# Kernel optimization log

Measured on AMD Instinct MI355X. Metric: run time of the kernel, lower is better.

The kernel has to match this reference:

```python
import jax, jax.numpy as jnp
import numpy as np
from jax import lax

N = 4096        # number of nodes (= number of hyperedges)
F_DIM = 256     # feature_dim
E_DIM = 128     # embed_dim
K = 9           # hardcoded k_neig in forward


def setup_inputs() -> dict:
    key = jax.random.key(0)
    ks = jax.random.split(key, 10)
    x = jax.random.normal(ks[0], (N, F_DIM), jnp.float32)
    # distance/similarity matrix; continuous values avoid argsort tie ambiguity
    XY_Adj = jax.random.uniform(ks[1], (N, N), jnp.float32)

    def unif(k, shape, fan_out):  # torch HGNN_conv init: U(-1/sqrt(out), 1/sqrt(out))
        s = 1.0 / np.sqrt(fan_out)
        return jax.random.uniform(k, shape, jnp.float32, -s, s)

    W10 = unif(ks[2], (F_DIM, E_DIM), E_DIM); b10 = unif(ks[3], (E_DIM,), E_DIM)
    W11 = unif(ks[4], (E_DIM, E_DIM), E_DIM); b11 = unif(ks[5], (E_DIM,), E_DIM)
    W20 = unif(ks[6], (E_DIM, E_DIM), E_DIM); b20 = unif(ks[7], (E_DIM,), E_DIM)
    W21 = unif(ks[8], (E_DIM, F_DIM), F_DIM); b21 = unif(ks[9], (F_DIM,), F_DIM)
    return {"x": x, "XY_Adj": XY_Adj,
            "W10": W10, "b10": b10, "W11": W11, "b11": b11,
            "W20": W20, "b20": b20, "W21": W21, "b21": b21}


def _build_G(dis, k):
    """Vectorized construct_H_with_KNN_from_distance + _generate_G_from_H.
    Picks the k LARGEST entries per row (original does reversed argsort),
    forces the center node into its own hyperedge, builds binary H [N,N]
    (rows=nodes, cols=hyperedges), then G = DV^-1/2 H DE^-1 H^T DV^-1/2 (W=I)."""
    n = dis.shape[0]
    centers = jnp.arange(n)
    dis = jnp.where(jnp.eye(n, dtype=bool), 0.0, dis)  # zero the diagonal
    _, idx = lax.top_k(dis, k)                         # [N, k] descending per row
    has_center = (idx == centers[:, None]).any(axis=1)
    idx = idx.at[:, k - 1].set(jnp.where(has_center, idx[:, k - 1], centers))
    H = jnp.zeros((n, n), dis.dtype).at[idx, centers[:, None]].set(1.0)
    DV = H.sum(axis=1)                                 # node degrees (>=1)
    DE = H.sum(axis=0)                                 # hyperedge degrees (=k)
    dv2 = DV ** -0.5
    left = dv2[:, None] * H * (1.0 / DE)[None, :]      # DV^-1/2 H DE^-1
    G = left @ (H.T * dv2[None, :])                    # ... H^T DV^-1/2
    return G


def _hgnn(x, G, W1, b1, W2, b2):
    # HGNN: relu(G(xW1+b1)) -> dropout (identity in eval) -> G(hW2+b2)
    h = jax.nn.relu(G @ (x @ W1 + b1))
    return G @ (h @ W2 + b2)


def reference(x, XY_Adj, W10, b10, W11, b11, W20, b20, W21, b21):
    G = _build_G(XY_Adj, K)
    x1 = jax.nn.relu(_hgnn(x, G, W10, b10, W11, b11))
    x2 = jax.nn.relu(_hgnn(x1, G, W20, b20, W21, b21))
    return (x, x1, x2)
```

## Files before the change

kernel.cpp:

```cpp
#include <hip/hip_runtime.h>

#define N_NODES 4096
#define KNN 9
#define CAPS 128
#define CAPE 32
#define THRESH 0.99f

__device__ __forceinline__ bool vi_greater(float av, int aj, float bv, int bj) {
  return (av > bv) || (av == bv && aj < bj);
}

__global__ void init_kernel(int* __restrict__ cur, int* __restrict__ elist) {
  int gid = blockIdx.x * blockDim.x + threadIdx.x;
  if (gid < N_NODES) cur[gid] = 0;
  for (int t = gid; t < N_NODES * CAPE; t += gridDim.x * blockDim.x)
    elist[t] = 0;
}

__global__ __launch_bounds__(256) void topk_kernel(const float* __restrict__ dis,
                                                   int* __restrict__ idx,
                                                   int* __restrict__ cur,
                                                   int* __restrict__ elist) {
  __shared__ float sval[4 * CAPS];
  __shared__ int   sidx[4 * CAPS];
  const int lane = threadIdx.x & 63;
  const int wv = threadIdx.x >> 6;
  const int row = blockIdx.x * 4 + wv;
  const float4* r4 = reinterpret_cast<const float4*>(dis + (size_t)row * N_NODES);
  float* wval = sval + wv * CAPS;
  int*   widx = sidx + wv * CAPS;
  const unsigned long long lmask = (1ull << lane) - 1;

  int n = 0;
#pragma unroll 4
  for (int t = 0; t < 16; ++t) {
    float4 f4 = r4[t * 64 + lane];
    float vals[4] = {f4.x, f4.y, f4.z, f4.w};
    int cb = (t * 64 + lane) * 4;
#pragma unroll
    for (int q = 0; q < 4; ++q) {
      int cc = cb + q;
      bool pred = (vals[q] > THRESH) && (cc != row);
      unsigned long long m = __ballot(pred);
      if (pred) {
        int p = n + __popcll(m & lmask);
        if (p < CAPS) { wval[p] = vals[q]; widx[p] = cc; }
      }
      n += __popcll(m);
    }
  }
  __syncthreads();

  int outj[KNN];
  if (n >= 8 && n <= CAPS) {
    float v0 = -3.0e38f, v1 = -3.0e38f;
    int c0 = 0x7fffffff, c1 = 0x7fffffff;
    if (lane < n)      { v0 = wval[lane];      c0 = widx[lane]; }
    if (lane + 64 < n) { v1 = wval[lane + 64]; c1 = widx[lane + 64]; }
#pragma unroll
    for (int rnd = 0; rnd < 8; ++rnd) {
      bool first = vi_greater(v0, c0, v1, c1);
      float mv = first ? v0 : v1;
      int   mc = first ? c0 : c1;
#pragma unroll
      for (int d = 1; d < 64; d <<= 1) {
        float ov = __shfl_xor(mv, d);
        int   oc = __shfl_xor(mc, d);
        if (vi_greater(ov, oc, mv, mc)) { mv = ov; mc = oc; }
      }
      outj[rnd] = mc;
      if (c0 == mc) v0 = -3.3e38f;
      if (c1 == mc) v1 = -3.3e38f;
    }
    outj[8] = row;
  } else {
    const float* r = dis + (size_t)row * N_NODES;
    float v[9]; int ji[9];
#pragma unroll
    for (int t = 0; t < 9; ++t) { v[t] = -3.0e38f; ji[t] = 0x7fffffff; }
    for (int t = 0; t < 64; ++t) {
      int cc = t * 64 + lane;
      float val = (cc == row) ? 0.0f : r[cc];
      if (vi_greater(val, cc, v[8], ji[8])) {
        v[8] = val; ji[8] = cc;
#pragma unroll
        for (int s = 8; s > 0; --s) {
          if (vi_greater(v[s], ji[s], v[s-1], ji[s-1])) {
            float tv = v[s]; v[s] = v[s-1]; v[s-1] = tv;
            int tj = ji[s]; ji[s] = ji[s-1]; ji[s-1] = tj;
          }
        }
      }
    }
    bool has_center = false;
#pragma unroll
    for (int rnd = 0; rnd < 9; ++rnd) {
      float mv = v[0]; int mj = ji[0];
#pragma unroll
      for (int d = 1; d < 64; d <<= 1) {
        float ov = __shfl_xor(mv, d);
        int   oj = __shfl_xor(mj, d);
        if (vi_greater(ov, oj, mv, mj)) { mv = ov; mj = oj; }
      }
      outj[rnd] = mj;
      has_center = has_center || (mj == row);
      if (ji[0] == mj) {
#pragma unroll
        for (int s = 0; s < 8; ++s) { v[s] = v[s+1]; ji[s] = ji[s+1]; }
        v[8] = -3.0e38f; ji[8] = 0x7fffffff;
      }
    }
    if (!has_center) outj[8] = row;
  }

  if (lane < KNN) {
    int j = outj[lane];
    idx[row * KNN + lane] = j;
    int p = atomicAdd(&cur[j], 1);
    if (p < CAPE) elist[j * CAPE + p] = row;
  }
}

template<int F>
__global__ __launch_bounds__(F) void edge_gather(const float* __restrict__ Y,
                                                 const int* __restrict__ idx,
                                                 const int* __restrict__ DV,
                                                 float* __restrict__ Z) {
  __shared__ int er[KNN];
  __shared__ float ew[KNN];
  int e = blockIdx.x;
  if (threadIdx.x < KNN) {
    int r = idx[e * KNN + threadIdx.x];
    er[threadIdx.x] = r;
    ew[threadIdx.x] = rsqrtf((float)DV[r]);
  }
  __syncthreads();
  int f = threadIdx.x;
  float acc = 0.f;
#pragma unroll
  for (int j = 0; j < KNN; ++j)
    acc = fmaf(ew[j], Y[(size_t)er[j] * F + f], acc);
  Z[(size_t)e * F + f] = acc * (1.0f / 9.0f);
}

template<int KD>
__device__ __forceinline__ float node_acc(const float* __restrict__ Z,
                                          const int* __restrict__ elist,
                                          int i, int f, int cnt) {
  const int4* el4 = reinterpret_cast<const int4*>(elist + i * CAPE);
  int4 ea = el4[0], eb = el4[1], ec = el4[2], ed = el4[3];
  int e1[16] = {ea.x, ea.y, ea.z, ea.w, eb.x, eb.y, eb.z, eb.w,
                ec.x, ec.y, ec.z, ec.w, ed.x, ed.y, ed.z, ed.w};
  float acc = 0.f;
#pragma unroll
  for (int j = 0; j < 16; ++j) {
    float m = (j < cnt) ? 1.0f : 0.0f;
    acc = fmaf(m, Z[(size_t)e1[j] * KD + f], acc);
  }
  for (int t = 16; t < cnt; ++t)
    acc += Z[(size_t)elist[i * CAPE + t] * KD + f];
  return acc;
}

template<int F>
__global__ __launch_bounds__(F) void node_gather(const float* __restrict__ Z,
                                                 const int* __restrict__ elist,
                                                 const int* __restrict__ DV,
                                                 float* __restrict__ out) {
  int i = blockIdx.x;
  int f = threadIdx.x;
  int cnt = DV[i]; if (cnt > CAPE) cnt = CAPE;
  float acc = node_acc<F>(Z, elist, i, f, cnt);
  out[(size_t)i * F + f] = fmaxf(acc * rsqrtf((float)DV[i]), 0.f);
}

template<int FO, bool WRITE_H>
__global__ __launch_bounds__(256) void node_gemm(const float* __restrict__ Z,
                                                 const int* __restrict__ elist,
                                                 const int* __restrict__ DV,
                                                 const float* __restrict__ W,
                                                 const float* __restrict__ bias,
                                                 float* __restrict__ P,
                                                 float* __restrict__ Hout) {
  constexpr int KD = 128;
  constexpr int ROWS = 4;
  constexpr int RPT = (FO == 128) ? 2 : 4;
  __shared__ float ylds[ROWS * KD];
  int m0 = blockIdx.x * ROWS;
#pragma unroll
  for (int c0 = 0; c0 < ROWS * KD; c0 += 256) {
    int cell = c0 + threadIdx.x;
    int rr = cell >> 7, f = cell & 127;
    int i = m0 + rr;
    int cnt = DV[i]; if (cnt > CAPE) cnt = CAPE;
    float acc = node_acc<KD>(Z, elist, i, f, cnt);
    acc = fmaxf(acc * rsqrtf((float)DV[i]), 0.f);
    ylds[cell] = acc;
    if (WRITE_H) Hout[(size_t)i * KD + f] = acc;
  }
  __syncthreads();
  const int f  = (FO == 128) ? (threadIdx.x & 127) : threadIdx.x;
  const int rb = (FO == 128) ? ((threadIdx.x >> 7) * 2) : 0;
  float acc[RPT];
#pragma unroll
  for (int rr = 0; rr < RPT; ++rr) acc[rr] = 0.f;
  for (int k = 0; k < KD; k += 4) {
    float w0 = W[(size_t)(k + 0) * FO + f];
    float w1 = W[(size_t)(k + 1) * FO + f];
    float w2 = W[(size_t)(k + 2) * FO + f];
    float w3 = W[(size_t)(k + 3) * FO + f];
#pragma unroll
    for (int rr = 0; rr < RPT; ++rr) {
      float4 y = *reinterpret_cast<const float4*>(&ylds[(rb + rr) * KD + k]);
      acc[rr] = fmaf(y.x, w0, fmaf(y.y, w1, fmaf(y.z, w2, fmaf(y.w, w3, acc[rr]))));
    }
  }
  float bb = bias[f];
#pragma unroll
  for (int rr = 0; rr < RPT; ++rr)
    P[(size_t)(m0 + rb + rr) * FO + f] = acc[rr] + bb;
}

template<bool COPY>
__global__ __launch_bounds__(256) void gemm_bias(const float* __restrict__ Y,
                                                 const float* __restrict__ W,
                                                 const float* __restrict__ bias,
                                                 float* __restrict__ P,
                                                 float* __restrict__ xcopy) {
  constexpr int KD = 256, FO = 128, ROWS = 4;
  __shared__ float ylds[ROWS * KD];
  int m0 = blockIdx.x * ROWS;
  for (int t = threadIdx.x; t < ROWS * KD / 4; t += 256) {
    float4 y4 = reinterpret_cast<const float4*>(Y + (size_t)m0 * KD)[t];
    reinterpret_cast<float4*>(ylds)[t] = y4;
    if (COPY) reinterpret_cast<float4*>(xcopy + (size_t)m0 * KD)[t] = y4;
  }
  __syncthreads();
  const int f  = threadIdx.x & 127;
  const int rb = (threadIdx.x >> 7) * 2;
  float acc[2] = {0.f, 0.f};
  for (int k = 0; k < KD; k += 4) {
    float w0 = W[(size_t)(k + 0) * FO + f];
    float w1 = W[(size_t)(k + 1) * FO + f];
    float w2 = W[(size_t)(k + 2) * FO + f];
    float w3 = W[(size_t)(k + 3) * FO + f];
#pragma unroll
    for (int rr = 0; rr < 2; ++rr) {
      float4 y = *reinterpret_cast<const float4*>(&ylds[(rb + rr) * KD + k]);
      acc[rr] = fmaf(y.x, w0, fmaf(y.y, w1, fmaf(y.z, w2, fmaf(y.w, w3, acc[rr]))));
    }
  }
  float bb = bias[f];
#pragma unroll
  for (int rr = 0; rr < 2; ++rr)
    P[(size_t)(m0 + rb + rr) * FO + f] = acc[rr] + bb;
}

extern "C" void kernel_launch(void* const* d_in, const int* in_sizes, int n_in,
                              void* d_out, int out_size, void* d_ws, size_t ws_size,
                              hipStream_t stream) {
  const float* x   = (const float*)d_in[0];
  const float* adj = (const float*)d_in[1];
  const float* W10 = (const float*)d_in[2];
  const float* b10 = (const float*)d_in[3];
  const float* W11 = (const float*)d_in[4];
  const float* b11 = (const float*)d_in[5];
  const float* W20 = (const float*)d_in[6];
  const float* b20 = (const float*)d_in[7];
  const float* W21 = (const float*)d_in[8];
  const float* b21 = (const float*)d_in[9];
  float* out = (float*)d_out;

  char* w = (char*)d_ws;
  int*   idx   = (int*)(w + 0);
  int*   cur   = (int*)(w + 147456);
  int*   elist = (int*)(w + 163840);
  float* bufP  = (float*)(w + 688128);
  float* bufZ  = (float*)(w + 4882432);

  float* x1out = out + (size_t)N_NODES * 256;
  float* x2out = out + (size_t)N_NODES * 256 + (size_t)N_NODES * 128;

  init_kernel<<<256, 256, 0, stream>>>(cur, elist);
  topk_kernel<<<N_NODES / 4, 256, 0, stream>>>(adj, idx, cur, elist);

  gemm_bias<true><<<N_NODES / 4, 256, 0, stream>>>(x, W10, b10, bufP, out);
  edge_gather<128><<<N_NODES, 128, 0, stream>>>(bufP, idx, cur, bufZ);
  node_gemm<128, false><<<N_NODES / 4, 256, 0, stream>>>(bufZ, elist, cur,
                                                         W11, b11, bufP, nullptr);
  edge_gather<128><<<N_NODES, 128, 0, stream>>>(bufP, idx, cur, bufZ);
  node_gemm<128, true><<<N_NODES / 4, 256, 0, stream>>>(bufZ, elist, cur,
                                                        W20, b20, bufP, x1out);
  edge_gather<128><<<N_NODES, 128, 0, stream>>>(bufP, idx, cur, bufZ);
  node_gemm<256, false><<<N_NODES / 4, 256, 0, stream>>>(bufZ, elist, cur,
                                                         W21, b21, bufP, nullptr);
  edge_gather<256><<<N_NODES, 256, 0, stream>>>(bufP, idx, cur, bufZ);
  node_gather<256><<<N_NODES, 256, 0, stream>>>(bufZ, elist, cur, x2out);
}
```

Before: 108.8 us.

## Scatter edge features into per-node slots instead of gathering via edge lists

Edge kernels now write each hyperedge's aggregated feature directly into a per-node slot buffer. Slot positions are precomputed in topk from the atomic counters. The node-side reduction then reads a contiguous slot range with no index indirection. The separate init kernel is dropped: the degree counter is zeroed inside the first GEMM, and the elist zeroing is removed entirely. The trade-off is roughly 9x more write traffic per layer and a far larger intermediate buffer. Node reads also always touch 16 slots, including unwritten ones, and these are masked by multiplying by zero, so stale non-finite values could corrupt results.

```diff
diff --git a/kernel.cpp b/kernel.cpp
--- a/kernel.cpp
+++ b/kernel.cpp
@@ -4,23 +4,17 @@
 #define KNN 9
 #define CAPS 128
 #define CAPE 32
+#define TRASH_SLOT (N_NODES * CAPE)
 #define THRESH 0.99f
 
 __device__ __forceinline__ bool vi_greater(float av, int aj, float bv, int bj) {
   return (av > bv) || (av == bv && aj < bj);
-}
-
-__global__ void init_kernel(int* __restrict__ cur, int* __restrict__ elist) {
-  int gid = blockIdx.x * blockDim.x + threadIdx.x;
-  if (gid < N_NODES) cur[gid] = 0;
-  for (int t = gid; t < N_NODES * CAPE; t += gridDim.x * blockDim.x)
-    elist[t] = 0;
 }
 
 __global__ __launch_bounds__(256) void topk_kernel(const float* __restrict__ dis,
                                                    int* __restrict__ idx,
                                                    int* __restrict__ cur,
-                                                   int* __restrict__ elist) {
+                                                   int* __restrict__ wslot) {
   __shared__ float sval[4 * CAPS];
   __shared__ int   sidx[4 * CAPS];
   const int lane = threadIdx.x & 63;
@@ -39,12 +33,11 @@
     int cb = (t * 64 + lane) * 4;
 #pragma unroll
     for (int q = 0; q < 4; ++q) {
-      int cc = cb + q;
-      bool pred = (vals[q] > THRESH) && (cc != row);
+      bool pred = (vals[q] > THRESH);
       unsigned long long m = __ballot(pred);
       if (pred) {
         int p = n + __popcll(m & lmask);
-        if (p < CAPS) { wval[p] = vals[q]; widx[p] = cc; }
+        if (p < CAPS) { wval[p] = vals[q]; widx[p] = cb + q; }
       }
       n += __popcll(m);
     }
@@ -52,11 +45,13 @@
   __syncthreads();
 
   int outj[KNN];
-  if (n >= 8 && n <= CAPS) {
+  if (n >= 9 && n <= CAPS) {
     float v0 = -3.0e38f, v1 = -3.0e38f;
     int c0 = 0x7fffffff, c1 = 0x7fffffff;
     if (lane < n)      { v0 = wval[lane];      c0 = widx[lane]; }
     if (lane + 64 < n) { v1 = wval[lane + 64]; c1 = widx[lane + 64]; }
+    if (c0 == row) v0 = -3.3e38f;
+    if (c1 == row) v1 = -3.3e38f;
 #pragma unroll
     for (int rnd = 0; rnd < 8; ++rnd) {
       bool first = vi_greater(v0, c0, v1, c1);
@@ -117,22 +112,25 @@
     int j = outj[lane];
     idx[row * KNN + lane] = j;
     int p = atomicAdd(&cur[j], 1);
-    if (p < CAPE) elist[j * CAPE + p] = row;
+    wslot[row * KNN + lane] = (p < CAPE) ? (j * CAPE + p) : TRASH_SLOT;
   }
 }
 
 template<int F>
-__global__ __launch_bounds__(F) void edge_gather(const float* __restrict__ Y,
-                                                 const int* __restrict__ idx,
-                                                 const int* __restrict__ DV,
-                                                 float* __restrict__ Z) {
+__global__ __launch_bounds__(F) void edge_scatter(const float* __restrict__ Y,
+                                                  const int* __restrict__ idx,
+                                                  const int* __restrict__ wslot,
+                                                  const int* __restrict__ DV,
+                                                  float* __restrict__ Zn) {
   __shared__ int er[KNN];
   __shared__ float ew[KNN];
+  __shared__ int ds[KNN];
   int e = blockIdx.x;
   if (threadIdx.x < KNN) {
     int r = idx[e * KNN + threadIdx.x];
     er[threadIdx.x] = r;
     ew[threadIdx.x] = rsqrtf((float)DV[r]);
+    ds[threadIdx.x] = wslot[e * KNN + threadIdx.x];
   }
   __syncthreads();
   int f = threadIdx.x;
@@ -140,43 +138,40 @@
 #pragma unroll
   for (int j = 0; j < KNN; ++j)
     acc = fmaf(ew[j], Y[(size_t)er[j] * F + f], acc);
-  Z[(size_t)e * F + f] = acc * (1.0f / 9.0f);
+  acc *= (1.0f / 9.0f);
+#pragma unroll
+  for (int j = 0; j < KNN; ++j)
+    Zn[(size_t)ds[j] * F + f] = acc;
 }
 
 template<int KD>
-__device__ __forceinline__ float node_acc(const float* __restrict__ Z,
-                                          const int* __restrict__ elist,
+__device__ __forceinline__ float node_acc(const float* __restrict__ Zn,
                                           int i, int f, int cnt) {
-  const int4* el4 = reinterpret_cast<const int4*>(elist + i * CAPE);
-  int4 ea = el4[0], eb = el4[1], ec = el4[2], ed = el4[3];
-  int e1[16] = {ea.x, ea.y, ea.z, ea.w, eb.x, eb.y, eb.z, eb.w,
-                ec.x, ec.y, ec.z, ec.w, ed.x, ed.y, ed.z, ed.w};
+  const float* base = Zn + (size_t)i * (CAPE * KD) + f;
   float acc = 0.f;
 #pragma unroll
-  for (int j = 0; j < 16; ++j) {
-    float m = (j < cnt) ? 1.0f : 0.0f;
-    acc = fmaf(m, Z[(size_t)e1[j] * KD + f], acc);
+  for (int t = 0; t < 16; ++t) {
+    float m = (t < cnt) ? 1.0f : 0.0f;
+    acc = fmaf(m, base[(size_t)t * KD], acc);
   }
   for (int t = 16; t < cnt; ++t)
-    acc += Z[(size_t)elist[i * CAPE + t] * KD + f];
+    acc += base[(size_t)t * KD];
   return acc;
 }
 
 template<int F>
-__global__ __launch_bounds__(F) void node_gather(const float* __restrict__ Z,
-                                                 const int* __restrict__ elist,
+__global__ __launch_bounds__(F) void node_gather(const float* __restrict__ Zn,
                                                  const int* __restrict__ DV,
                                                  float* __restrict__ out) {
   int i = blockIdx.x;
   int f = threadIdx.x;
   int cnt = DV[i]; if (cnt > CAPE) cnt = CAPE;
-  float acc = node_acc<F>(Z, elist, i, f, cnt);
+  float acc = node_acc<F>(Zn, i, f, cnt);
   out[(size_t)i * F + f] = fmaxf(acc * rsqrtf((float)DV[i]), 0.f);
 }
 
 template<int FO, bool WRITE_H>
-__global__ __launch_bounds__(256) void node_gemm(const float* __restrict__ Z,
-                                                 const int* __restrict__ elist,
+__global__ __launch_bounds__(256) void node_gemm(const float* __restrict__ Zn,
                                                  const int* __restrict__ DV,
                                                  const float* __restrict__ W,
                                                  const float* __restrict__ bias,
@@ -193,7 +188,7 @@
     int rr = cell >> 7, f = cell & 127;
     int i = m0 + rr;
     int cnt = DV[i]; if (cnt > CAPE) cnt = CAPE;
-    float acc = node_acc<KD>(Z, elist, i, f, cnt);
+    float acc = node_acc<KD>(Zn, i, f, cnt);
     acc = fmaxf(acc * rsqrtf((float)DV[i]), 0.f);
     ylds[cell] = acc;
     if (WRITE_H) Hout[(size_t)i * KD + f] = acc;
@@ -221,19 +216,21 @@
     P[(size_t)(m0 + rb + rr) * FO + f] = acc[rr] + bb;
 }
 
-template<bool COPY>
-__global__ __launch_bounds__(256) void gemm_bias(const float* __restrict__ Y,
-                                                 const float* __restrict__ W,
-                                                 const float* __restrict__ bias,
-                                                 float* __restrict__ P,
-                                                 float* __restrict__ xcopy) {
+__global__ __launch_bounds__(256) void gemm_first(const float* __restrict__ Y,
+                                                  const float* __restrict__ W,
+                                                  const float* __restrict__ bias,
+                                                  float* __restrict__ P,
+                                                  float* __restrict__ xcopy,
+                                                  int* __restrict__ cur) {
   constexpr int KD = 256, FO = 128, ROWS = 4;
   __shared__ float ylds[ROWS * KD];
+  int gid = blockIdx.x * 256 + threadIdx.x;
+  if (gid < N_NODES) cur[gid] = 0;
   int m0 = blockIdx.x * ROWS;
   for (int t = threadIdx.x; t < ROWS * KD / 4; t += 256) {
     float4 y4 = reinterpret_cast<const float4*>(Y + (size_t)m0 * KD)[t];
     reinterpret_cast<float4*>(ylds)[t] = y4;
-    if (COPY) reinterpret_cast<float4*>(xcopy + (size_t)m0 * KD)[t] = y4;
+    reinterpret_cast<float4*>(xcopy + (size_t)m0 * KD)[t] = y4;
   }
   __syncthreads();
   const int f  = threadIdx.x & 127;
@@ -273,27 +270,26 @@
 
   char* w = (char*)d_ws;
   int*   idx   = (int*)(w + 0);
-  int*   cur   = (int*)(w + 147456);
-  int*   elist = (int*)(w + 163840);
-  float* bufP  = (float*)(w + 688128);
-  float* bufZ  = (float*)(w + 4882432);
+  int*   wslot = (int*)(w + 147456);
+  int*   cur   = (int*)(w + 294912);
+  float* bufP  = (float*)(w + 311296);
+  float* Zn    = (float*)(w + 4505600);
 
   float* x1out = out + (size_t)N_NODES * 256;
   float* x2out = out + (size_t)N_NODES * 256 + (size_t)N_NODES * 128;
 
-  init_kernel<<<256, 256, 0, stream>>>(cur, elist);
-  topk_kernel<<<N_NODES / 4, 256, 0, stream>>>(adj, idx, cur, elist);
-
-  gemm_bias<true><<<N_NODES / 4, 256, 0, stream>>>(x, W10, b10, bufP, out);
-  edge_gather<128><<<N_NODES, 128, 0, stream>>>(bufP, idx, cur, bufZ);
-  node_gemm<128, false><<<N_NODES / 4, 256, 0, stream>>>(bufZ, elist, cur,
-                                                         W11, b11, bufP, nullptr);
-  edge_gather<128><<<N_NODES, 128, 0, stream>>>(bufP, idx, cur, bufZ);
-  node_gemm<128, true><<<N_NODES / 4, 256, 0, stream>>>(bufZ, elist, cur,
-                                                        W20, b20, bufP, x1out);
-  edge_gather<128><<<N_NODES, 128, 0, stream>>>(bufP, idx, cur, bufZ);
-  node_gemm<256, false><<<N_NODES / 4, 256, 0, stream>>>(bufZ, elist, cur,
-                                                         W21, b21, bufP, nullptr);
-  edge_gather<256><<<N_NODES, 256, 0, stream>>>(bufP, idx, cur, bufZ);
-  node_gather<256><<<N_NODES, 256, 0, stream>>>(bufZ, elist, cur, x2out);
-}
+  gemm_first<<<N_NODES / 4, 256, 0, stream>>>(x, W10, b10, bufP, out, cur);
+  topk_kernel<<<N_NODES / 4, 256, 0, stream>>>(adj, idx, cur, wslot);
+
+  edge_scatter<128><<<N_NODES, 128, 0, stream>>>(bufP, idx, wslot, cur, Zn);
+  node_gemm<128, false><<<N_NODES / 4, 256, 0, stream>>>(Zn, cur, W11, b11,
+                                                         bufP, nullptr);
+  edge_scatter<128><<<N_NODES, 128, 0, stream>>>(bufP, idx, wslot, cur, Zn);
+  node_gemm<128, true><<<N_NODES / 4, 256, 0, stream>>>(Zn, cur, W20, b20,
+                                                        bufP, x1out);
+  edge_scatter<128><<<N_NODES, 128, 0, stream>>>(bufP, idx, wslot, cur, Zn);
+  node_gemm<256, false><<<N_NODES / 4, 256, 0, stream>>>(Zn, cur, W21, b21,
+                                                         bufP, nullptr);
+  edge_scatter<256><<<N_NODES, 256, 0, stream>>>(bufP, idx, wslot, cur, Zn);
+  node_gather<256><<<N_NODES, 256, 0, stream>>>(Zn, cur, x2out);
+}
```

Result: slower. 121.1 us (+11.2%).

## Reassociate HGNN propagation before weights and fuse edge/node gathers into one pass

Applied to the files above, without the earlier changes.

The code rewrites G(hW+b) as (Gh)W + (G·1)b. Propagation then runs on the narrower 128-wide features before each weight GEMM, with the bias scaled by a per-row weight sum. The separate edge-gather and node-gather kernels become one two-hop gather per node, using edge and member indices staged in shared memory. The elist init kernel is dropped, and zeroing the counters is folded into the first GEMM, so the launch count falls from 11 to 6. In exchange, each node now re-gathers about 9×degree feature rows instead of reusing per-edge partial sums, which raises redundant global and L2 read traffic.

```diff
diff --git a/kernel.cpp b/kernel.cpp
--- a/kernel.cpp
+++ b/kernel.cpp
@@ -4,17 +4,48 @@
 #define KNN 9
 #define CAPS 128
 #define CAPE 32
+#define NSTG 16
 #define THRESH 0.99f
 
 __device__ __forceinline__ bool vi_greater(float av, int aj, float bv, int bj) {
   return (av > bv) || (av == bv && aj < bj);
 }
 
-__global__ void init_kernel(int* __restrict__ cur, int* __restrict__ elist) {
-  int gid = blockIdx.x * blockDim.x + threadIdx.x;
+__global__ __launch_bounds__(256) void gemm_first(const float* __restrict__ Y,
+                                                  const float* __restrict__ W,
+                                                  const float* __restrict__ bias,
+                                                  float* __restrict__ P,
+                                                  float* __restrict__ xcopy,
+                                                  int* __restrict__ cur) {
+  constexpr int KD = 256, FO = 128, ROWS = 4;
+  __shared__ float ylds[ROWS * KD];
+  int gid = blockIdx.x * 256 + threadIdx.x;
   if (gid < N_NODES) cur[gid] = 0;
-  for (int t = gid; t < N_NODES * CAPE; t += gridDim.x * blockDim.x)
-    elist[t] = 0;
+  int m0 = blockIdx.x * ROWS;
+  for (int t = threadIdx.x; t < ROWS * KD / 4; t += 256) {
+    float4 y4 = reinterpret_cast<const float4*>(Y + (size_t)m0 * KD)[t];
+    reinterpret_cast<float4*>(ylds)[t] = y4;
+    reinterpret_cast<float4*>(xcopy + (size_t)m0 * KD)[t] = y4;
+  }
+  __syncthreads();
+  const int f  = threadIdx.x & 127;
+  const int rb = (threadIdx.x >> 7) * 2;
+  float acc[2] = {0.f, 0.f};
+  for (int k = 0; k < KD; k += 4) {
+    float w0 = W[(size_t)(k + 0) * FO + f];
+    float w1 = W[(size_t)(k + 1) * FO + f];
+    float w2 = W[(size_t)(k + 2) * FO + f];
+    float w3 = W[(size_t)(k + 3) * FO + f];
+#pragma unroll
+    for (int rr = 0; rr < 2; ++rr) {
+      float4 y = *reinterpret_cast<const float4*>(&ylds[(rb + rr) * KD + k]);
+      acc[rr] = fmaf(y.x, w0, fmaf(y.y, w1, fmaf(y.z, w2, fmaf(y.w, w3, acc[rr]))));
+    }
+  }
+  float bb = bias[f];
+#pragma unroll
+  for (int rr = 0; rr < 2; ++rr)
+    P[(size_t)(m0 + rb + rr) * FO + f] = acc[rr] + bb;
 }
 
 __global__ __launch_bounds__(256) void topk_kernel(const float* __restrict__ dis,
@@ -121,139 +152,132 @@
   }
 }
 
-template<int F>
-__global__ __launch_bounds__(F) void edge_gather(const float* __restrict__ Y,
-                                                 const int* __restrict__ idx,
-                                                 const int* __restrict__ DV,
-                                                 float* __restrict__ Z) {
-  __shared__ int er[KNN];
-  __shared__ float ew[KNN];
-  int e = blockIdx.x;
-  if (threadIdx.x < KNN) {
-    int r = idx[e * KNN + threadIdx.x];
-    er[threadIdx.x] = r;
-    ew[threadIdx.x] = rsqrtf((float)DV[r]);
-  }
-  __syncthreads();
-  int f = threadIdx.x;
-  float acc = 0.f;
-#pragma unroll
-  for (int j = 0; j < KNN; ++j)
-    acc = fmaf(ew[j], Y[(size_t)er[j] * F + f], acc);
-  Z[(size_t)e * F + f] = acc * (1.0f / 9.0f);
-}
-
-template<int KD>
-__device__ __forceinline__ float node_acc(const float* __restrict__ Z,
+struct GnodeLds {
+  int2  srw[4][NSTG * KNN];
+  int   se[4][NSTG];
+  float sdvi[4];
+  int   scnt[4];
+  float ylds[4 * 128];
+  float rlds[4];
+};
+
+__device__ __forceinline__ void gnode_stage(GnodeLds& L, int m0, int tid,
+                                            const int* __restrict__ idx,
+                                            const int* __restrict__ elist,
+                                            const int* __restrict__ DV) {
+  if (tid < 4 * NSTG) {
+    int rr = tid >> 4, t = tid & (NSTG - 1);
+    int i = m0 + rr;
+    int dv = DV[i];
+    int cnt = dv < NSTG ? dv : NSTG;
+    int e = elist[i * CAPE + t];
+    L.se[rr][t] = (t < cnt) ? e : -1;
+    if (t == 0) {
+      L.sdvi[rr] = rsqrtf((float)dv);
+      L.scnt[rr] = dv < CAPE ? dv : CAPE;
+    }
+  }
+  __syncthreads();
+  for (int q = tid; q < 4 * NSTG * KNN; q += 256) {
+    int rr = q / (NSTG * KNN), rem = q % (NSTG * KNN);
+    int e = L.se[rr][rem / KNN];
+    int r = (e >= 0) ? idx[e * KNN + rem % KNN] : 0;
+    float wgt = (e >= 0) ? rsqrtf((float)DV[r]) : 0.f;
+    L.srw[rr][rem] = make_int2(r, __float_as_int(wgt));
+  }
+  __syncthreads();
+}
+
+__device__ __forceinline__ void gnode_acc(const GnodeLds& L, int m0, int rr,
+                                          int f, const float* __restrict__ Y,
+                                          const int* __restrict__ idx,
                                           const int* __restrict__ elist,
-                                          int i, int f, int cnt) {
-  const int4* el4 = reinterpret_cast<const int4*>(elist + i * CAPE);
-  int4 ea = el4[0], eb = el4[1], ec = el4[2], ed = el4[3];
-  int e1[16] = {ea.x, ea.y, ea.z, ea.w, eb.x, eb.y, eb.z, eb.w,
-                ec.x, ec.y, ec.z, ec.w, ed.x, ed.y, ed.z, ed.w};
-  float acc = 0.f;
-#pragma unroll
-  for (int j = 0; j < 16; ++j) {
-    float m = (j < cnt) ? 1.0f : 0.0f;
-    acc = fmaf(m, Z[(size_t)e1[j] * KD + f], acc);
-  }
-  for (int t = 16; t < cnt; ++t)
-    acc += Z[(size_t)elist[i * CAPE + t] * KD + f];
-  return acc;
-}
-
-template<int F>
-__global__ __launch_bounds__(F) void node_gather(const float* __restrict__ Z,
-                                                 const int* __restrict__ elist,
-                                                 const int* __restrict__ DV,
-                                                 float* __restrict__ out) {
-  int i = blockIdx.x;
-  int f = threadIdx.x;
-  int cnt = DV[i]; if (cnt > CAPE) cnt = CAPE;
-  float acc = node_acc<F>(Z, elist, i, f, cnt);
-  out[(size_t)i * F + f] = fmaxf(acc * rsqrtf((float)DV[i]), 0.f);
-}
-
-template<int FO, bool WRITE_H>
-__global__ __launch_bounds__(256) void node_gemm(const float* __restrict__ Z,
-                                                 const int* __restrict__ elist,
-                                                 const int* __restrict__ DV,
-                                                 const float* __restrict__ W,
-                                                 const float* __restrict__ bias,
-                                                 float* __restrict__ P,
-                                                 float* __restrict__ Hout) {
-  constexpr int KD = 128;
-  constexpr int ROWS = 4;
+                                          const int* __restrict__ DV,
+                                          float& Sv, float& rv) {
+  float acc = 0.f, racc = 0.f;
+#pragma unroll 12
+  for (int q = 0; q < NSTG * KNN; ++q) {
+    int2 p = L.srw[rr][q];
+    float wq = __int_as_float(p.y);
+    acc = fmaf(wq, Y[(size_t)p.x * 128 + f], acc);
+    racc += wq;
+  }
+  int cntf = L.scnt[rr];
+  for (int t = NSTG; t < cntf; ++t) {
+    int e = elist[(m0 + rr) * CAPE + t];
+#pragma unroll
+    for (int j = 0; j < KNN; ++j) {
+      int r = idx[e * KNN + j];
+      float wq = rsqrtf((float)DV[r]);
+      acc = fmaf(wq, Y[(size_t)r * 128 + f], acc);
+      racc += wq;
+    }
+  }
+  float s = L.sdvi[rr] * (1.0f / 9.0f);
+  Sv = acc * s;
+  rv = racc * s;
+}
+
+__global__ __launch_bounds__(256) void gnode_relu(const float* __restrict__ Y,
+                                                  const int* __restrict__ idx,
+                                                  const int* __restrict__ elist,
+                                                  const int* __restrict__ DV,
+                                                  float* __restrict__ H) {
+  __shared__ GnodeLds L;
+  int m0 = blockIdx.x * 4, tid = threadIdx.x;
+  gnode_stage(L, m0, tid, idx, elist, DV);
+#pragma unroll
+  for (int c0 = 0; c0 < 512; c0 += 256) {
+    int cell = c0 + tid, rr = cell >> 7, f = cell & 127;
+    float Sv, rv;
+    gnode_acc(L, m0, rr, f, Y, idx, elist, DV, Sv, rv);
+    H[(size_t)(m0 + rr) * 128 + f] = fmaxf(Sv, 0.f);
+  }
+}
+
+template<int FO>
+__global__ __launch_bounds__(256) void gnode_gemm(const float* __restrict__ Y,
+                                                  const int* __restrict__ idx,
+                                                  const int* __restrict__ elist,
+                                                  const int* __restrict__ DV,
+                                                  const float* __restrict__ W,
+                                                  const float* __restrict__ bias,
+                                                  float* __restrict__ P) {
   constexpr int RPT = (FO == 128) ? 2 : 4;
-  __shared__ float ylds[ROWS * KD];
-  int m0 = blockIdx.x * ROWS;
-#pragma unroll
-  for (int c0 = 0; c0 < ROWS * KD; c0 += 256) {
-    int cell = c0 + threadIdx.x;
-    int rr = cell >> 7, f = cell & 127;
-    int i = m0 + rr;
-    int cnt = DV[i]; if (cnt > CAPE) cnt = CAPE;
-    float acc = node_acc<KD>(Z, elist, i, f, cnt);
-    acc = fmaxf(acc * rsqrtf((float)DV[i]), 0.f);
-    ylds[cell] = acc;
-    if (WRITE_H) Hout[(size_t)i * KD + f] = acc;
-  }
-  __syncthreads();
-  const int f  = (FO == 128) ? (threadIdx.x & 127) : threadIdx.x;
-  const int rb = (FO == 128) ? ((threadIdx.x >> 7) * 2) : 0;
+  __shared__ GnodeLds L;
+  int m0 = blockIdx.x * 4, tid = threadIdx.x;
+  gnode_stage(L, m0, tid, idx, elist, DV);
+#pragma unroll
+  for (int c0 = 0; c0 < 512; c0 += 256) {
+    int cell = c0 + tid, rr = cell >> 7, f = cell & 127;
+    float Sv, rv;
+    gnode_acc(L, m0, rr, f, Y, idx, elist, DV, Sv, rv);
+    L.ylds[cell] = Sv;
+    if (f == 0) L.rlds[rr] = rv;
+  }
+  __syncthreads();
+  const int f  = (FO == 128) ? (tid & 127) : tid;
+  const int rb = (FO == 128) ? ((tid >> 7) * 2) : 0;
   float acc[RPT];
 #pragma unroll
   for (int rr = 0; rr < RPT; ++rr) acc[rr] = 0.f;
-  for (int k = 0; k < KD; k += 4) {
+  for (int k = 0; k < 128; k += 4) {
     float w0 = W[(size_t)(k + 0) * FO + f];
     float w1 = W[(size_t)(k + 1) * FO + f];
     float w2 = W[(size_t)(k + 2) * FO + f];
     float w3 = W[(size_t)(k + 3) * FO + f];
 #pragma unroll
     for (int rr = 0; rr < RPT; ++rr) {
-      float4 y = *reinterpret_cast<const float4*>(&ylds[(rb + rr) * KD + k]);
+      float4 y = *reinterpret_cast<const float4*>(&L.ylds[(rb + rr) * 128 + k]);
       acc[rr] = fmaf(y.x, w0, fmaf(y.y, w1, fmaf(y.z, w2, fmaf(y.w, w3, acc[rr]))));
     }
   }
   float bb = bias[f];
 #pragma unroll
-  for (int rr = 0; rr < RPT; ++rr)
-    P[(size_t)(m0 + rb + rr) * FO + f] = acc[rr] + bb;
-}
-
-template<bool COPY>
-__global__ __launch_bounds__(256) void gemm_bias(const float* __restrict__ Y,
-                                                 const float* __restrict__ W,
-                                                 const float* __restrict__ bias,
-                                                 float* __restrict__ P,
-                                                 float* __restrict__ xcopy) {
-  constexpr int KD = 256, FO = 128, ROWS = 4;
-  __shared__ float ylds[ROWS * KD];
-  int m0 = blockIdx.x * ROWS;
-  for (int t = threadIdx.x; t < ROWS * KD / 4; t += 256) {
-    float4 y4 = reinterpret_cast<const float4*>(Y + (size_t)m0 * KD)[t];
-    reinterpret_cast<float4*>(ylds)[t] = y4;
-    if (COPY) reinterpret_cast<float4*>(xcopy + (size_t)m0 * KD)[t] = y4;
-  }
-  __syncthreads();
-  const int f  = threadIdx.x & 127;
-  const int rb = (threadIdx.x >> 7) * 2;
-  float acc[2] = {0.f, 0.f};
-  for (int k = 0; k < KD; k += 4) {
-    float w0 = W[(size_t)(k + 0) * FO + f];
-    float w1 = W[(size_t)(k + 1) * FO + f];
-    float w2 = W[(size_t)(k + 2) * FO + f];
-    float w3 = W[(size_t)(k + 3) * FO + f];
-#pragma unroll
-    for (int rr = 0; rr < 2; ++rr) {
-      float4 y = *reinterpret_cast<const float4*>(&ylds[(rb + rr) * KD + k]);
-      acc[rr] = fmaf(y.x, w0, fmaf(y.y, w1, fmaf(y.z, w2, fmaf(y.w, w3, acc[rr]))));
-    }
-  }
-  float bb = bias[f];
-#pragma unroll
-  for (int rr = 0; rr < 2; ++rr)
-    P[(size_t)(m0 + rb + rr) * FO + f] = acc[rr] + bb;
+  for (int rr = 0; rr < RPT; ++rr) {
+    float rv = L.rlds[rb + rr];
+    P[(size_t)(m0 + rb + rr) * FO + f] = fmaxf(fmaf(rv, bb, acc[rr]), 0.f);
+  }
 }
 
 extern "C" void kernel_launch(void* const* d_in, const int* in_sizes, int n_in,
@@ -276,24 +300,18 @@
   int*   cur   = (int*)(w + 147456);
   int*   elist = (int*)(w + 163840);
   float* bufP  = (float*)(w + 688128);
-  float* bufZ  = (float*)(w + 4882432);
+  float* bufH  = (float*)(w + 688128 + 2097152);
 
   float* x1out = out + (size_t)N_NODES * 256;
-  float* x2out = out + (size_t)N_NODES * 256 + (size_t)N_NODES * 128;
-
-  init_kernel<<<256, 256, 0, stream>>>(cur, elist);
+  float* x2out = x1out + (size_t)N_NODES * 128;
+
+  gemm_first<<<N_NODES / 4, 256, 0, stream>>>(x, W10, b10, bufP, out, cur);
   topk_kernel<<<N_NODES / 4, 256, 0, stream>>>(adj, idx, cur, elist);
-
-  gemm_bias<true><<<N_NODES / 4, 256, 0, stream>>>(x, W10, b10, bufP, out);
-  edge_gather<128><<<N_NODES, 128, 0, stream>>>(bufP, idx, cur, bufZ);
-  node_gemm<128, false><<<N_NODES / 4, 256, 0, stream>>>(bufZ, elist, cur,
-                                                         W11, b11, bufP, nullptr);
-  edge_gather<128><<<N_NODES, 128, 0, stream>>>(bufP, idx, cur, bufZ);
-  node_gemm<128, true><<<N_NODES / 4, 256, 0, stream>>>(bufZ, elist, cur,
-                                                        W20, b20, bufP, x1out);
-  edge_gather<128><<<N_NODES, 128, 0, stream>>>(bufP, idx, cur, bufZ);
-  node_gemm<256, false><<<N_NODES / 4, 256, 0, stream>>>(bufZ, elist, cur,
-                                                         W21, b21, bufP, nullptr);
-  edge_gather<256><<<N_NODES, 256, 0, stream>>>(bufP, idx, cur, bufZ);
-  node_gather<256><<<N_NODES, 256, 0, stream>>>(bufZ, elist, cur, x2out);
-}
+  gnode_relu<<<N_NODES / 4, 256, 0, stream>>>(bufP, idx, elist, cur, bufH);
+  gnode_gemm<128><<<N_NODES / 4, 256, 0, stream>>>(bufH, idx, elist, cur,
+                                                   W11, b11, x1out);
+  gnode_gemm<128><<<N_NODES / 4, 256, 0, stream>>>(x1out, idx, elist, cur,
+                                                   W20, b20, bufH);
+  gnode_gemm<256><<<N_NODES / 4, 256, 0, stream>>>(bufH, idx, elist, cur,
+                                                   W21, b21, x2out);
+}
```

Result: slower. 125.4 us (+15.2%).

## Fuse init, top-k and first GEMM into one launch; split elist build; double node_gemm rows

Applied to the files above, without the earlier changes.

Merges the init kernel, the top-k selection and the first x@W10 GEMM into a single launch, with blocks split by index between the GEMM and the top-k work, so the two independent stages run concurrently. Hyperedge list construction moves to a separate small kernel after top-k, and masked elist reads are clamped so elist no longer needs zero-initialisation. node_gemm now processes 8 rows per block instead of 4, halving grid size and reusing each W load across more rows. This removes a launch and the elist memset, at the cost of an extra launch for build_elist and fewer, heavier blocks in node_gemm.

```diff
diff --git a/kernel.cpp b/kernel.cpp
--- a/kernel.cpp
+++ b/kernel.cpp
@@ -5,120 +5,150 @@
 #define CAPS 128
 #define CAPE 32
 #define THRESH 0.99f
+#define GEMMB 1024
 
 __device__ __forceinline__ bool vi_greater(float av, int aj, float bv, int bj) {
   return (av > bv) || (av == bv && aj < bj);
 }
 
-__global__ void init_kernel(int* __restrict__ cur, int* __restrict__ elist) {
-  int gid = blockIdx.x * blockDim.x + threadIdx.x;
-  if (gid < N_NODES) cur[gid] = 0;
-  for (int t = gid; t < N_NODES * CAPE; t += gridDim.x * blockDim.x)
-    elist[t] = 0;
-}
-
-__global__ __launch_bounds__(256) void topk_kernel(const float* __restrict__ dis,
-                                                   int* __restrict__ idx,
-                                                   int* __restrict__ cur,
-                                                   int* __restrict__ elist) {
-  __shared__ float sval[4 * CAPS];
-  __shared__ int   sidx[4 * CAPS];
-  const int lane = threadIdx.x & 63;
-  const int wv = threadIdx.x >> 6;
-  const int row = blockIdx.x * 4 + wv;
-  const float4* r4 = reinterpret_cast<const float4*>(dis + (size_t)row * N_NODES);
-  float* wval = sval + wv * CAPS;
-  int*   widx = sidx + wv * CAPS;
-  const unsigned long long lmask = (1ull << lane) - 1;
-
-  int n = 0;
+__global__ __launch_bounds__(256) void s0_kernel(const float* __restrict__ x,
+                                                 const float* __restrict__ adj,
+                                                 const float* __restrict__ W10,
+                                                 const float* __restrict__ b10,
+                                                 float* __restrict__ P,
+                                                 float* __restrict__ xcopy,
+                                                 int* __restrict__ cur,
+                                                 int* __restrict__ idx) {
+  __shared__ float sf[1024];
+  __shared__ int   si[512];
+  const int tid = threadIdx.x;
+
+  if (blockIdx.x < GEMMB) {
+    int gid = blockIdx.x * 256 + tid;
+    if (gid < N_NODES) cur[gid] = 0;
+    int m0 = blockIdx.x * 4;
+    {
+      float4 y4 = reinterpret_cast<const float4*>(x + (size_t)m0 * 256)[tid];
+      reinterpret_cast<float4*>(sf)[tid] = y4;
+      reinterpret_cast<float4*>(xcopy + (size_t)m0 * 256)[tid] = y4;
+    }
+    __syncthreads();
+    const int f  = tid & 127;
+    const int rb = (tid >> 7) * 2;
+    float a0 = 0.f, a1 = 0.f;
+    for (int k = 0; k < 256; k += 4) {
+      float w0 = W10[(k + 0) * 128 + f];
+      float w1 = W10[(k + 1) * 128 + f];
+      float w2 = W10[(k + 2) * 128 + f];
+      float w3 = W10[(k + 3) * 128 + f];
+      float4 y0 = *reinterpret_cast<const float4*>(&sf[(rb + 0) * 256 + k]);
+      float4 y1 = *reinterpret_cast<const float4*>(&sf[(rb + 1) * 256 + k]);
+      a0 = fmaf(y0.x, w0, fmaf(y0.y, w1, fmaf(y0.z, w2, fmaf(y0.w, w3, a0))));
+      a1 = fmaf(y1.x, w0, fmaf(y1.y, w1, fmaf(y1.z, w2, fmaf(y1.w, w3, a1))));
+    }
+    float bb = b10[f];
+    P[(size_t)(m0 + rb + 0) * 128 + f] = a0 + bb;
+    P[(size_t)(m0 + rb + 1) * 128 + f] = a1 + bb;
+  } else {
+    const int lane = tid & 63, wv = tid >> 6;
+    const int row = (blockIdx.x - GEMMB) * 4 + wv;
+    const float4* r4 = reinterpret_cast<const float4*>(adj + (size_t)row * N_NODES);
+    float* wval = sf + wv * CAPS;
+    int*   widx = si + wv * CAPS;
+    const unsigned long long lmask = (1ull << lane) - 1;
+
+    int n = 0;
 #pragma unroll 4
-  for (int t = 0; t < 16; ++t) {
-    float4 f4 = r4[t * 64 + lane];
-    float vals[4] = {f4.x, f4.y, f4.z, f4.w};
-    int cb = (t * 64 + lane) * 4;
-#pragma unroll
-    for (int q = 0; q < 4; ++q) {
-      int cc = cb + q;
-      bool pred = (vals[q] > THRESH) && (cc != row);
-      unsigned long long m = __ballot(pred);
-      if (pred) {
-        int p = n + __popcll(m & lmask);
-        if (p < CAPS) { wval[p] = vals[q]; widx[p] = cc; }
-      }
-      n += __popcll(m);
-    }
-  }
-  __syncthreads();
-
-  int outj[KNN];
-  if (n >= 8 && n <= CAPS) {
-    float v0 = -3.0e38f, v1 = -3.0e38f;
-    int c0 = 0x7fffffff, c1 = 0x7fffffff;
-    if (lane < n)      { v0 = wval[lane];      c0 = widx[lane]; }
-    if (lane + 64 < n) { v1 = wval[lane + 64]; c1 = widx[lane + 64]; }
-#pragma unroll
-    for (int rnd = 0; rnd < 8; ++rnd) {
-      bool first = vi_greater(v0, c0, v1, c1);
-      float mv = first ? v0 : v1;
-      int   mc = first ? c0 : c1;
-#pragma unroll
-      for (int d = 1; d < 64; d <<= 1) {
-        float ov = __shfl_xor(mv, d);
-        int   oc = __shfl_xor(mc, d);
-        if (vi_greater(ov, oc, mv, mc)) { mv = ov; mc = oc; }
-      }
-      outj[rnd] = mc;
-      if (c0 == mc) v0 = -3.3e38f;
-      if (c1 == mc) v1 = -3.3e38f;
-    }
-    outj[8] = row;
-  } else {
-    const float* r = dis + (size_t)row * N_NODES;
-    float v[9]; int ji[9];
-#pragma unroll
-    for (int t = 0; t < 9; ++t) { v[t] = -3.0e38f; ji[t] = 0x7fffffff; }
-    for (int t = 0; t < 64; ++t) {
-      int cc = t * 64 + lane;
-      float val = (cc == row) ? 0.0f : r[cc];
-      if (vi_greater(val, cc, v[8], ji[8])) {
-        v[8] = val; ji[8] = cc;
-#pragma unroll
-        for (int s = 8; s > 0; --s) {
-          if (vi_greater(v[s], ji[s], v[s-1], ji[s-1])) {
-            float tv = v[s]; v[s] = v[s-1]; v[s-1] = tv;
-            int tj = ji[s]; ji[s] = ji[s-1]; ji[s-1] = tj;
+    for (int t = 0; t < 16; ++t) {
+      float4 f4 = r4[t * 64 + lane];
+      float vals[4] = {f4.x, f4.y, f4.z, f4.w};
+      int cb = (t * 64 + lane) * 4;
+#pragma unroll
+      for (int q = 0; q < 4; ++q) {
+        int cc = cb + q;
+        bool pred = (vals[q] > THRESH) && (cc != row);
+        unsigned long long m = __ballot(pred);
+        if (pred) {
+          int p = n + __popcll(m & lmask);
+          if (p < CAPS) { wval[p] = vals[q]; widx[p] = cc; }
+        }
+        n += __popcll(m);
+      }
+    }
+    __syncthreads();
+
+    int outj[KNN];
+    if (n >= 8 && n <= CAPS) {
+      float v0 = -3.0e38f, v1 = -3.0e38f;
+      int c0 = 0x7fffffff, c1 = 0x7fffffff;
+      if (lane < n)      { v0 = wval[lane];      c0 = widx[lane]; }
+      if (lane + 64 < n) { v1 = wval[lane + 64]; c1 = widx[lane + 64]; }
+#pragma unroll
+      for (int rnd = 0; rnd < 8; ++rnd) {
+        bool first = vi_greater(v0, c0, v1, c1);
+        float mv = first ? v0 : v1;
+        int   mc = first ? c0 : c1;
+#pragma unroll
+        for (int d = 1; d < 64; d <<= 1) {
+          float ov = __shfl_xor(mv, d);
+          int   oc = __shfl_xor(mc, d);
+          if (vi_greater(ov, oc, mv, mc)) { mv = ov; mc = oc; }
+        }
+        outj[rnd] = mc;
+        if (c0 == mc) v0 = -3.3e38f;
+        if (c1 == mc) v1 = -3.3e38f;
+      }
+      outj[8] = row;
+    } else {
+      const float* r = adj + (size_t)row * N_NODES;
+      float v[9]; int ji[9];
+#pragma unroll
+      for (int t = 0; t < 9; ++t) { v[t] = -3.0e38f; ji[t] = 0x7fffffff; }
+      for (int t = 0; t < 64; ++t) {
+        int cc = t * 64 + lane;
+        float val = (cc == row) ? 0.0f : r[cc];
+        if (vi_greater(val, cc, v[8], ji[8])) {
+          v[8] = val; ji[8] = cc;
+#pragma unroll
+          for (int s = 8; s > 0; --s) {
+            if (vi_greater(v[s], ji[s], v[s-1], ji[s-1])) {
+              float tv = v[s]; v[s] = v[s-1]; v[s-1] = tv;
+              int tj = ji[s]; ji[s] = ji[s-1]; ji[s-1] = tj;
+            }
           }
         }
       }
-    }
-    bool has_center = false;
-#pragma unroll
-    for (int rnd = 0; rnd < 9; ++rnd) {
-      float mv = v[0]; int mj = ji[0];
-#pragma unroll
-      for (int d = 1; d < 64; d <<= 1) {
-        float ov = __shfl_xor(mv, d);
-        int   oj = __shfl_xor(mj, d);
-        if (vi_greater(ov, oj, mv, mj)) { mv = ov; mj = oj; }
-      }
-      outj[rnd] = mj;
-      has_center = has_center || (mj == row);
-      if (ji[0] == mj) {
-#pragma unroll
-        for (int s = 0; s < 8; ++s) { v[s] = v[s+1]; ji[s] = ji[s+1]; }
-        v[8] = -3.0e38f; ji[8] = 0x7fffffff;
-      }
-    }
-    if (!has_center) outj[8] = row;
-  }
-
-  if (lane < KNN) {
-    int j = outj[lane];
-    idx[row * KNN + lane] = j;
-    int p = atomicAdd(&cur[j], 1);
-    if (p < CAPE) elist[j * CAPE + p] = row;
-  }
+      bool has_center = false;
+#pragma unroll
+      for (int rnd = 0; rnd < 9; ++rnd) {
+        float mv = v[0]; int mj = ji[0];
+#pragma unroll
+        for (int d = 1; d < 64; d <<= 1) {
+          float ov = __shfl_xor(mv, d);
+          int   oj = __shfl_xor(mj, d);
+          if (vi_greater(ov, oj, mv, mj)) { mv = ov; mj = oj; }
+        }
+        outj[rnd] = mj;
+        has_center = has_center || (mj == row);
+        if (ji[0] == mj) {
+#pragma unroll
+          for (int s = 0; s < 8; ++s) { v[s] = v[s+1]; ji[s] = ji[s+1]; }
+          v[8] = -3.0e38f; ji[8] = 0x7fffffff;
+        }
+      }
+      if (!has_center) outj[8] = row;
+    }
+    if (lane < KNN) idx[row * KNN + lane] = outj[lane];
+  }
+}
+
+__global__ void build_elist(const int* __restrict__ idx, int* __restrict__ cur,
+                            int* __restrict__ elist) {
+  int t = blockIdx.x * blockDim.x + threadIdx.x;
+  if (t >= N_NODES * KNN) return;
+  int node = idx[t];
+  int p = atomicAdd(&cur[node], 1);
+  if (p < CAPE) elist[node * CAPE + p] = t / KNN;
 }
 
 template<int F>
@@ -155,7 +185,7 @@
 #pragma unroll
   for (int j = 0; j < 16; ++j) {
     float m = (j < cnt) ? 1.0f : 0.0f;
-    acc = fmaf(m, Z[(size_t)e1[j] * KD + f], acc);
+    acc = fmaf(m, Z[(size_t)(e1[j] & (N_NODES - 1)) * KD + f], acc);
   }
   for (int t = 16; t < cnt; ++t)
     acc += Z[(size_t)elist[i * CAPE + t] * KD + f];
@@ -183,8 +213,8 @@
                                                  float* __restrict__ P,
                                                  float* __restrict__ Hout) {
   constexpr int KD = 128;
-  constexpr int ROWS = 4;
-  constexpr int RPT = (FO == 128) ? 2 : 4;
+  constexpr int ROWS = 8;
+  constexpr int RPT = (FO == 128) ? 4 : 8;
   __shared__ float ylds[ROWS * KD];
   int m0 = blockIdx.x * ROWS;
 #pragma unroll
@@ -200,7 +230,7 @@
   }
   __syncthreads();
   const int f  = (FO == 128) ? (threadIdx.x & 127) : threadIdx.x;
-  const int rb = (FO == 128) ? ((threadIdx.x >> 7) * 2) : 0;
+  const int rb = (FO == 128) ? ((threadIdx.x >> 7) * 4) : 0;
   float acc[RPT];
 #pragma unroll
   for (int rr = 0; rr < RPT; ++rr) acc[rr] = 0.f;
@@ -218,41 +248,6 @@
   float bb = bias[f];
 #pragma unroll
   for (int rr = 0; rr < RPT; ++rr)
-    P[(size_t)(m0 + rb + rr) * FO + f] = acc[rr] + bb;
-}
-
-template<bool COPY>
-__global__ __launch_bounds__(256) void gemm_bias(const float* __restrict__ Y,
-                                                 const float* __restrict__ W,
-                                                 const float* __restrict__ bias,
-                                                 float* __restrict__ P,
-                                                 float* __restrict__ xcopy) {
-  constexpr int KD = 256, FO = 128, ROWS = 4;
-  __shared__ float ylds[ROWS * KD];
-  int m0 = blockIdx.x * ROWS;
-  for (int t = threadIdx.x; t < ROWS * KD / 4; t += 256) {
-    float4 y4 = reinterpret_cast<const float4*>(Y + (size_t)m0 * KD)[t];
-    reinterpret_cast<float4*>(ylds)[t] = y4;
-    if (COPY) reinterpret_cast<float4*>(xcopy + (size_t)m0 * KD)[t] = y4;
-  }
-  __syncthreads();
-  const int f  = threadIdx.x & 127;
-  const int rb = (threadIdx.x >> 7) * 2;
-  float acc[2] = {0.f, 0.f};
-  for (int k = 0; k < KD; k += 4) {
-    float w0 = W[(size_t)(k + 0) * FO + f];
-    float w1 = W[(size_t)(k + 1) * FO + f];
-    float w2 = W[(size_t)(k + 2) * FO + f];
-    float w3 = W[(size_t)(k + 3) * FO + f];
-#pragma unroll
-    for (int rr = 0; rr < 2; ++rr) {
-      float4 y = *reinterpret_cast<const float4*>(&ylds[(rb + rr) * KD + k]);
-      acc[rr] = fmaf(y.x, w0, fmaf(y.y, w1, fmaf(y.z, w2, fmaf(y.w, w3, acc[rr]))));
-    }
-  }
-  float bb = bias[f];
-#pragma unroll
-  for (int rr = 0; rr < 2; ++rr)
     P[(size_t)(m0 + rb + rr) * FO + f] = acc[rr] + bb;
 }
 
@@ -279,20 +274,19 @@
   float* bufZ  = (float*)(w + 4882432);
 
   float* x1out = out + (size_t)N_NODES * 256;
-  float* x2out = out + (size_t)N_NODES * 256 + (size_t)N_NODES * 128;
-
-  init_kernel<<<256, 256, 0, stream>>>(cur, elist);
-  topk_kernel<<<N_NODES / 4, 256, 0, stream>>>(adj, idx, cur, elist);
-
-  gemm_bias<true><<<N_NODES / 4, 256, 0, stream>>>(x, W10, b10, bufP, out);
+  float* x2out = x1out + (size_t)N_NODES * 128;
+
+  s0_kernel<<<2 * GEMMB, 256, 0, stream>>>(x, adj, W10, b10, bufP, out, cur, idx);
+  build_elist<<<(N_NODES * KNN + 255) / 256, 256, 0, stream>>>(idx, cur, elist);
+
   edge_gather<128><<<N_NODES, 128, 0, stream>>>(bufP, idx, cur, bufZ);
-  node_gemm<128, false><<<N_NODES / 4, 256, 0, stream>>>(bufZ, elist, cur,
+  node_gemm<128, false><<<N_NODES / 8, 256, 0, stream>>>(bufZ, elist, cur,
                                                          W11, b11, bufP, nullptr);
   edge_gather<128><<<N_NODES, 128, 0, stream>>>(bufP, idx, cur, bufZ);
-  node_gemm<128, true><<<N_NODES / 4, 256, 0, stream>>>(bufZ, elist, cur,
+  node_gemm<128, true><<<N_NODES / 8, 256, 0, stream>>>(bufZ, elist, cur,
                                                         W20, b20, bufP, x1out);
   edge_gather<128><<<N_NODES, 128, 0, stream>>>(bufP, idx, cur, bufZ);
-  node_gemm<256, false><<<N_NODES / 4, 256, 0, stream>>>(bufZ, elist, cur,
+  node_gemm<256, false><<<N_NODES / 8, 256, 0, stream>>>(bufZ, elist, cur,
                                                          W21, b21, bufP, nullptr);
   edge_gather<256><<<N_NODES, 256, 0, stream>>>(bufP, idx, cur, bufZ);
   node_gather<256><<<N_NODES, 256, 0, stream>>>(bufZ, elist, cur, x2out);
```

Result: faster. 98.37 us (-9.6%).
